# Kernel optimization log

Hardware: AMD Instinct MI355X
Metric: run time of the kernel (lower is better)

## Reference

```python
import jax, jax.numpy as jnp
import numpy as np

S, B, D = 2048, 2, 2048      # seq, batch, hidden  (x is [S, B, D])
H, KV, HD = 16, 4, 128        # n_head, n_kv_head, head_dim
N_REP = H // KV               # GQA repeat factor
THETA = 10000.0


def setup_inputs() -> dict:
    key = jax.random.key(0)
    ks = jax.random.split(key, 5)
    sc = 1.0 / np.sqrt(D)
    x = jax.random.normal(ks[0], (S, B, D), jnp.float32)
    Wq = jax.random.normal(ks[1], (D, H * HD), jnp.float32) * sc
    Wk = jax.random.normal(ks[2], (D, KV * HD), jnp.float32) * sc
    Wv = jax.random.normal(ks[3], (D, KV * HD), jnp.float32) * sc
    Wo = jax.random.normal(ks[4], (H * HD, D), jnp.float32) * sc
    return {"x": x, "Wq": Wq, "Wk": Wk, "Wv": Wv, "Wo": Wo}


def _rope_cos_sin(seq_len, dim, theta):
    inv_freq = 1.0 / (theta ** (jnp.arange(0, dim, 2, dtype=jnp.float32) / dim))
    t = jnp.arange(seq_len, dtype=jnp.float32)
    freqs = jnp.outer(t, inv_freq)                  # [S, dim/2]
    emb = jnp.concatenate([freqs, freqs], axis=-1)  # [S, dim]
    return jnp.cos(emb), jnp.sin(emb)


def _rotate_half(u):
    u1, u2 = jnp.split(u, 2, axis=-1)
    return jnp.concatenate([-u2, u1], axis=-1)


def reference(x, Wq, Wk, Wv, Wo):
    # projections (torch Linear without bias; W stored as [in, out] here)
    q = (x @ Wq).reshape(S, B, H, HD)
    k = (x @ Wk).reshape(S, B, KV, HD)
    v = (x @ Wv).reshape(S, B, KV, HD)

    # RoPE (full rotary, partial_rotary_factor == 1.0)
    cos, sin = _rope_cos_sin(S, HD, THETA)
    cos = cos[:, None, None, :]  # [S,1,1,HD] broadcasts over B, heads
    sin = sin[:, None, None, :]
    q = q * cos + _rotate_half(q) * sin
    k = k * cos + _rotate_half(k) * sin

    # GQA: repeat_interleave kv heads to match query heads
    k = jnp.repeat(k, N_REP, axis=2)
    v = jnp.repeat(v, N_REP, axis=2)

    # [S,B,H,HD] -> [B,H,S,HD]
    q = q.transpose(1, 2, 0, 3)
    k = k.transpose(1, 2, 0, 3)
    v = v.transpose(1, 2, 0, 3)

    # causal SDPA (dropout_p = 0 in eval)
    scale = 1.0 / np.sqrt(HD)
    scores = jnp.einsum('bhqd,bhkd->bhqk', q, k) * scale
    causal = jnp.tril(jnp.ones((S, S), dtype=bool))
    scores = jnp.where(causal, scores, jnp.finfo(scores.dtype).min)
    probs = jax.nn.softmax(scores, axis=-1)
    out = jnp.einsum('bhqk,bhkd->bhqd', probs, v)

    # [B,H,S,HD] -> [S,B,D], then output projection
    out = out.transpose(2, 0, 1, 3).reshape(S, B, D)
    return out @ Wo
```

## Files before the change

### kernel.cpp

```cpp
#include <hip/hip_runtime.h>
#include <hip/hip_bf16.h>
#include <cstdint>
#include <math.h>

#define S_LEN   2048
#define B_SZ    2
#define D_MODEL 2048
#define NH      16
#define NKV     4
#define HD      128
#define ROWS    (S_LEN * B_SZ)
#define NQKV    3072
#define SCALE   0.08838834764831845f

typedef __attribute__((ext_vector_type(8))) short short8;
typedef __attribute__((ext_vector_type(4))) float f32x4;

__device__ __forceinline__ short f2bf(float f) {
  union { float f; unsigned u; } v; v.f = f;
  unsigned r = v.u + 0x7fffu + ((v.u >> 16) & 1u);
  return (short)(r >> 16);
}
__device__ __forceinline__ float bf2f(short x) {
  union { unsigned u; float f; } v;
  v.u = ((unsigned)(unsigned short)x) << 16;
  return v.f;
}

__device__ __forceinline__ void async16(const short* g, short* l) {
  __builtin_amdgcn_global_load_lds(
      (const __attribute__((address_space(1))) void*)(uintptr_t)(const void*)g,
      (__attribute__((address_space(3))) void*)(uintptr_t)(void*)l,
      16, 0, 0);
}

template<int N> __device__ __forceinline__ void vm_wait() {
  asm volatile("s_waitcnt vmcnt(%0)" :: "n"(N) : "memory");
}

__global__ void cvt_bf16_kernel(const float* __restrict__ src, short* __restrict__ dst, int n4) {
  int t = blockIdx.x * blockDim.x + threadIdx.x;
  if (t >= n4) return;
  float4 v = ((const float4*)src)[t];
  short4 o;
  o.x = f2bf(v.x); o.y = f2bf(v.y); o.z = f2bf(v.z); o.w = f2bf(v.w);
  *(short4*)(dst + (size_t)t * 4) = o;
}

__global__ void wtrans_qkv_kernel(const float* __restrict__ Wq,
                                  const float* __restrict__ Wk,
                                  const float* __restrict__ Wv,
                                  short* __restrict__ dst) {
  __shared__ float tile[32][33];
  const int bx = blockIdx.x;
  const float* src;
  int Ndim, n0, drow;
  if (bx < 64)      { src = Wq; Ndim = 2048; n0 = bx * 32;        drow = n0; }
  else if (bx < 80) { src = Wk; Ndim = 512;  n0 = (bx - 64) * 32; drow = 2048 + n0; }
  else              { src = Wv; Ndim = 512;  n0 = (bx - 80) * 32; drow = 2560 + n0; }
  const int k0 = blockIdx.y * 32;
  for (int r = threadIdx.y; r < 32; r += 8)
    tile[r][threadIdx.x] = src[(size_t)(k0 + r) * Ndim + n0 + threadIdx.x];
  __syncthreads();
  for (int r = threadIdx.y; r < 32; r += 8)
    dst[(size_t)(drow + r) * 2048 + k0 + threadIdx.x] = f2bf(tile[threadIdx.x][r]);
}

__global__ void wtrans_kernel(const float* __restrict__ src, short* __restrict__ dst,
                              int Kdim, int Ndim) {
  __shared__ float tile[32][33];
  int n0 = blockIdx.x * 32, k0 = blockIdx.y * 32;
  for (int r = threadIdx.y; r < 32; r += 8)
    tile[r][threadIdx.x] = src[(size_t)(k0 + r) * Ndim + n0 + threadIdx.x];
  __syncthreads();
  for (int r = threadIdx.y; r < 32; r += 8)
    dst[(size_t)(n0 + r) * Kdim + k0 + threadIdx.x] = f2bf(tile[threadIdx.x][r]);
}

template<int BM, int BF16OUT>
__global__ __launch_bounds__(512, 2) void gemm3_kernel(const short* __restrict__ A,
    const short* __restrict__ Bt, void* __restrict__ Cv, int N, int K) {
  constexpr int MGRP  = BM / 16;
  constexpr int MI    = BM / 32;
  constexpr int NP    = MI / 2;
  constexpr int BCALLS = 4;
  constexpr int ACALLS = MGRP / 4;
  constexpr int CALLS = BCALLS + ACALLS;
  constexpr int BS_SH = 16384;
  constexpr int BUFSH = BS_SH + MGRP * 1024;
  __shared__ alignas(16) short lds[2 * BUFSH];

  const int tid  = threadIdx.x;
  const int w    = tid >> 6, lane = tid & 63;
  const int quad = lane >> 4, lr = lane & 15;
  const int wm   = w >> 2, wn = w & 3;

  const int nwg = gridDim.x;
  const int id  = (blockIdx.x & 7) * (nwg >> 3) + (blockIdx.x >> 3);
  const int nbx = N >> 8;
  const int bx = id % nbx, by = id / nbx;
  const int m0 = by * BM, n0 = bx * 256;

  const short* gsrc[CALLS];
  int dsts[CALLS];
#pragma unroll
  for (int c = 0; c < CALLS; ++c) {
    if (c < BCALLS) {
      const int sb = c * 8 + w, ng = sb >> 1, kk = sb & 1;
      gsrc[c] = Bt + (size_t)(n0 + ng * 16 + lr) * K + kk * 32 + quad * 8;
      dsts[c] = sb * 512;
    } else {
      const int p = c - BCALLS;
      const int mg = (w >> 2) * (MGRP / 2) + 2 * p + ((w >> 1) & 1), kk = w & 1;
      gsrc[c] = A + (size_t)(m0 + mg * 16 + lr) * K + kk * 32 + quad * 8;
      dsts[c] = BS_SH + (p * 8 + w) * 512;
    }
  }

  f32x4 acc[MI][4];
#pragma unroll
  for (int i = 0; i < MI; ++i)
#pragma unroll
    for (int j = 0; j < 4; ++j) acc[i][j] = (f32x4){0.f, 0.f, 0.f, 0.f};

  auto stage = [&](int t, int c) {
    async16(gsrc[c] + (size_t)t * 64, lds + (t & 1) * BUFSH + dsts[c]);
  };

  const int NT = K >> 6;
#pragma unroll
  for (int c = 0; c < CALLS; ++c) stage(0, c);
  if (BM == 256) vm_wait<3>(); else vm_wait<1>();
  __builtin_amdgcn_s_barrier();
  asm volatile("" ::: "memory");

  for (int t = 0; t < NT; ++t) {
    const short* lb = lds + (t & 1) * BUFSH;
    const bool pre = (t + 1) < NT;
    short8 b[4][2];
#pragma unroll
    for (int p = 0; p < NP; ++p) {
      if (p == 0) {
#pragma unroll
        for (int j = 0; j < 4; ++j)
#pragma unroll
          for (int kk = 0; kk < 2; ++kk)
            b[j][kk] = *(const short8*)(lb + ((wn * 4 + j) * 2 + kk) * 512 + lane * 8);
      }
      short8 a[2][2];
#pragma unroll
      for (int e = 0; e < 2; ++e)
#pragma unroll
        for (int kk = 0; kk < 2; ++kk)
          a[e][kk] = *(const short8*)(lb + BS_SH + (p * 8 + (wm * 2 + e) * 2 + kk) * 512 + lane * 8);
      if (pre) {
        if (NP == 4) { stage(t + 1, 2 * p); stage(t + 1, 2 * p + 1); }
        else         { stage(t + 1, 3 * p); stage(t + 1, 3 * p + 1); stage(t + 1, 3 * p + 2); }
      }
      asm volatile("" ::: "memory");
      __builtin_amdgcn_s_barrier();
      asm volatile("s_waitcnt lgkmcnt(0)" ::: "memory");
      __builtin_amdgcn_s_setprio(1);
#pragma unroll
      for (int kk = 0; kk < 2; ++kk)
#pragma unroll
        for (int e = 0; e < 2; ++e)
#pragma unroll
          for (int j = 0; j < 4; ++j)
            acc[2 * p + e][j] = __builtin_amdgcn_mfma_f32_16x16x32_bf16(a[e][kk], b[j][kk], acc[2 * p + e][j], 0, 0, 0);
      __builtin_amdgcn_s_setprio(0);
      if (pre) {
        if (NP == 4) {
          if (p == 0) vm_wait<4>(); else if (p == 1) vm_wait<5>();
          else if (p == 2) vm_wait<6>(); else vm_wait<3>();
        } else {
          if (p == 0) vm_wait<3>(); else vm_wait<1>();
        }
      } else {
        if (NP == 4) {
          if (p == 0) vm_wait<2>(); else if (p == 1) vm_wait<1>();
          else if (p == 2) vm_wait<0>();
        } else {
          if (p == 0) vm_wait<0>();
        }
      }
      asm volatile("" ::: "memory");
      __builtin_amdgcn_s_barrier();
      asm volatile("" ::: "memory");
    }
  }

#pragma unroll
  for (int i = 0; i < MI; ++i) {
    const int row = m0 + wm * (BM / 2) + i * 16 + quad * 4;
#pragma unroll
    for (int j = 0; j < 4; ++j) {
      const int col = n0 + wn * 64 + j * 16 + lr;
#pragma unroll
      for (int r = 0; r < 4; ++r) {
        const float v = acc[i][j][r];
        if (BF16OUT) ((short*)Cv)[(size_t)(row + r) * N + col] = f2bf(v);
        else         ((float*)Cv)[(size_t)(row + r) * N + col] = v;
      }
    }
  }
}

__global__ void rope_kernel(const short* __restrict__ QKVb, short* __restrict__ Qb,
                            short* __restrict__ Kpack) {
  const int head = blockIdx.y;
  const int t = blockIdx.x * blockDim.x + threadIdx.x;
  const int i = t & 63;
  const int row = t >> 6;
  const int s = row >> 1;
  const int b = row & 1;
  float inv_freq = __expf(-(float)i * (1.0f / 64.0f) * 9.210340371976184f);
  float ang = (float)s * inv_freq;
  float sn, cs;
  __sincosf(ang, &sn, &cs);
  if (head < NH) {
    const short* p = QKVb + (size_t)row * NQKV + head * HD;
    float v1 = bf2f(p[i]), v2 = bf2f(p[i + 64]);
    short* q = Qb + ((size_t)(b * NH + head) * S_LEN + s) * HD;
    q[i]      = f2bf((v1 * cs - v2 * sn) * SCALE);
    q[i + 64] = f2bf((v2 * cs + v1 * sn) * SCALE);
  } else {
    const int kv = head - NH;
    const short* p = QKVb + (size_t)row * NQKV + NH * HD + kv * HD;
    float v1 = bf2f(p[i]), v2 = bf2f(p[i + 64]);
    float k1 = v1 * cs - v2 * sn;
    float k2 = v2 * cs + v1 * sn;
    short* kp = Kpack + (size_t)(b * NKV + kv) * S_LEN * HD;
    const int tile = s >> 4, lrr = s & 15;
    const int d1 = i, d2 = i + 64;
    kp[(size_t)((tile * 4 + (d1 >> 5)) * 64 + ((d1 >> 3) & 3) * 16 + lrr) * 8 + (d1 & 7)] = f2bf(k1);
    kp[(size_t)((tile * 4 + (d2 >> 5)) * 64 + ((d2 >> 3) & 3) * 16 + lrr) * 8 + (d2 & 7)] = f2bf(k2);
  }
}

__global__ void vpack_kernel(const short* __restrict__ QKVb, short* __restrict__ Vpack) {
  __shared__ short tile[32][136];
  const int tid = threadIdx.x;
  const int chunk = blockIdx.x & 63, stream = blockIdx.x >> 6;
  const int b = stream >> 2, kv = stream & 3;
  const int vcol = NH * HD + NKV * HD + kv * HD;
  {
    const int r = tid >> 3, c = (tid & 7) * 16;
    const short* src = QKVb + (size_t)((chunk * 32 + r) * B_SZ + b) * NQKV + vcol + c;
    *(short8*)(&tile[r][c])     = *(const short8*)(src);
    *(short8*)(&tile[r][c + 8]) = *(const short8*)(src + 8);
  }
  __syncthreads();
  const int wave = tid >> 6, lane = tid & 63, quad = lane >> 4, lr = lane & 15;
  short* dst = Vpack + (size_t)stream * HD * S_LEN + chunk * 4096 + lane * 8;
#pragma unroll
  for (int k = 0; k < 2; ++k) {
    const int dt = wave + k * 4;
    short8 v;
#pragma unroll
    for (int j = 0; j < 8; ++j) v[j] = tile[quad * 8 + j][dt * 16 + lr];
    *(short8*)(dst + dt * 512) = v;
  }
}

#define PSP 72

template<bool MASK>
__device__ __forceinline__ void attn_iter64(
    const short* __restrict__ Ks, const short* __restrict__ Vs,
    short* __restrict__ Psw, const short8 qf[4], int kv0, int nt, int qlim,
    int quad, int lr, int lane, f32x4 o[8], float& m_i, float& l_i)
{
  const int lane_off = lane * 8;
  f32x4 sc[4];
#pragma unroll
  for (int t = 0; t < 4; ++t) {
    if (t < nt) {
      const short* kp = Ks + t * 2048 + lane_off;
      f32x4 s = (f32x4){0.f, 0.f, 0.f, 0.f};
#pragma unroll
      for (int c = 0; c < 4; ++c) {
        short8 kf = *(const short8*)(kp + c * 512);
        s = __builtin_amdgcn_mfma_f32_16x16x32_bf16(kf, qf[c], s, 0, 0, 0);
      }
      sc[t] = s;
    } else {
      sc[t] = (f32x4){-3.0e38f, -3.0e38f, -3.0e38f, -3.0e38f};
    }
  }
  if (MASK) {
#pragma unroll
    for (int t = 0; t < 4; ++t)
#pragma unroll
      for (int r = 0; r < 4; ++r)
        if (kv0 + t * 16 + quad * 4 + r > qlim) sc[t][r] = -3.0e38f;
  }
  float mb = -3.0e38f;
#pragma unroll
  for (int t = 0; t < 4; ++t)
#pragma unroll
    for (int r = 0; r < 4; ++r) mb = fmaxf(mb, sc[t][r]);
  mb = fmaxf(mb, __shfl_xor(mb, 16, 64));
  mb = fmaxf(mb, __shfl_xor(mb, 32, 64));
  const float mnew = fmaxf(m_i, mb);
  const float alpha = __expf(m_i - mnew);
  m_i = mnew;
  float rs = 0.f;
#pragma unroll
  for (int t = 0; t < 4; ++t) {
    float p0 = __expf(sc[t][0] - mnew);
    float p1 = __expf(sc[t][1] - mnew);
    float p2 = __expf(sc[t][2] - mnew);
    float p3 = __expf(sc[t][3] - mnew);
    rs += (p0 + p1) + (p2 + p3);
    __hip_bfloat162 pk01 = __float22bfloat162_rn(make_float2(p0, p1));
    __hip_bfloat162 pk23 = __float22bfloat162_rn(make_float2(p2, p3));
    __hip_bfloat162* pd = (__hip_bfloat162*)(Psw + lr * PSP + t * 16 + quad * 4);
    pd[0] = pk01;
    pd[1] = pk23;
  }
  rs += __shfl_xor(rs, 16, 64);
  rs += __shfl_xor(rs, 32, 64);
  l_i = l_i * alpha + rs;
#pragma unroll
  for (int n = 0; n < 8; ++n)
#pragma unroll
    for (int r = 0; r < 4; ++r) o[n][r] *= alpha;
  short8 pb0 = *(const short8*)(Psw + lr * PSP + quad * 8);
#pragma unroll
  for (int dt = 0; dt < 8; ++dt) {
    short8 vf = *(const short8*)(Vs + dt * 512 + lane_off);
    o[dt] = __builtin_amdgcn_mfma_f32_16x16x32_bf16(vf, pb0, o[dt], 0, 0, 0);
  }
  if (!MASK || nt > 2) {
    short8 pb1 = *(const short8*)(Psw + lr * PSP + 32 + quad * 8);
#pragma unroll
    for (int dt = 0; dt < 8; ++dt) {
      short8 vf = *(const short8*)(Vs + 4096 + dt * 512 + lane_off);
      o[dt] = __builtin_amdgcn_mfma_f32_16x16x32_bf16(vf, pb1, o[dt], 0, 0, 0);
    }
  }
}

__global__ __launch_bounds__(256) void attn_kernel(const short* __restrict__ Qb,
    const short* __restrict__ Kpack, const short* __restrict__ Vpack,
    short* __restrict__ Ob) {
  __shared__ alignas(16) short Ks[2][64 * HD];
  __shared__ alignas(16) short Vs[2][64 * HD];
  __shared__ alignas(16) short Ps[4][16 * PSP];
  const int tid = threadIdx.x, wave = tid >> 6, lane = tid & 63;
  const int quad = lane >> 4, lr = lane & 15;
  const int bid = blockIdx.x;
  const int sid  = bid & 7;
  const int hsub = (bid >> 3) & 3;
  const int qg   = 31 - (bid >> 5);
  const int b = sid >> 2, kvh = sid & 3;
  const int h = kvh * 4 + hsub;
  const int qw = (qg * 4 + wave) * 16;

  const short* Qp  = Qb    + ((size_t)(b * NH + h) * S_LEN + qw) * HD;
  const short* Kpk = Kpack + (size_t)(b * NKV + kvh) * S_LEN * HD;
  const short* Vpk = Vpack + (size_t)(b * NKV + kvh) * HD * S_LEN;
  short* Psw = &Ps[wave][0];

  short8 qf[4];
#pragma unroll
  for (int c = 0; c < 4; ++c)
    qf[c] = *(const short8*)(Qp + lr * HD + c * 32 + quad * 8);

  f32x4 o[8];
#pragma unroll
  for (int n = 0; n < 8; ++n) o[n] = (f32x4){0.f, 0.f, 0.f, 0.f};
  float m_i = -3.0e38f, l_i = 0.f;

  auto stage_kv = [&](int it) {
    const int buf = it & 1;
    const int kv0 = it * 64;
    const short* gk = Kpk + (size_t)kv0 * HD;
    const short* gv = Vpk + (size_t)(kv0 >> 5) * 4096;
#pragma unroll
    for (int k = 0; k < 4; ++k) {
      const int off = (wave * 4 + k) * 512;
      async16(gk + off + lane * 8, &Ks[buf][off]);
      async16(gv + off + lane * 8, &Vs[buf][off]);
    }
  };

  const int qlim = qw + lr;
  stage_kv(0);
  for (int it = 0; it <= qg; ++it) {
    __syncthreads();
    if (it < qg) stage_kv(it + 1);
    const int buf = it & 1;
    if (it < qg)
      attn_iter64<false>(Ks[buf], Vs[buf], Psw, qf, it * 64, 4, qlim, quad, lr, lane, o, m_i, l_i);
    else
      attn_iter64<true>(Ks[buf], Vs[buf], Psw, qf, it * 64, wave + 1, qlim, quad, lr, lane, o, m_i, l_i);
  }

  const float invl = 1.0f / l_i;
  short* op = Ob + ((size_t)(qw + lr) * B_SZ + b) * D_MODEL + h * HD + quad * 4;
#pragma unroll
  for (int dt = 0; dt < 8; ++dt) {
    short4 ov;
    ov.x = f2bf(o[dt][0] * invl);
    ov.y = f2bf(o[dt][1] * invl);
    ov.z = f2bf(o[dt][2] * invl);
    ov.w = f2bf(o[dt][3] * invl);
    *(short4*)(op + dt * 16) = ov;
  }
}

extern "C" void kernel_launch(void* const* d_in, const int* in_sizes, int n_in,
                              void* d_out, int out_size, void* d_ws, size_t ws_size,
                              hipStream_t stream) {
  (void)in_sizes; (void)n_in; (void)out_size; (void)ws_size;
  const float* x  = (const float*)d_in[0];
  const float* Wq = (const float*)d_in[1];
  const float* Wk = (const float*)d_in[2];
  const float* Wv = (const float*)d_in[3];
  const float* Wo = (const float*)d_in[4];
  float* out = (float*)d_out;
  char* ws = (char*)d_ws;

  short* Wqkv_t = (short*)(ws);
  short* xb     = (short*)(ws + 12582912);
  short* Qb     = (short*)(ws);
  short* Kpack  = (short*)(ws + 16777216);
  short* Vpack  = (short*)(ws + 25165824);
  short* QKVb   = (short*)(ws + 29360128);
  short* Ob     = (short*)(ws + 29360128);
  short* Wo_t   = (short*)(ws + 54525952);

  dim3 tblk(32, 8);

  cvt_bf16_kernel<<<(ROWS * D_MODEL / 4 + 255) / 256, 256, 0, stream>>>(x, xb, ROWS * D_MODEL / 4);
  wtrans_qkv_kernel<<<dim3(96, 64), tblk, 0, stream>>>(Wq, Wk, Wv, Wqkv_t);
  wtrans_kernel<<<dim3(64, 64), tblk, 0, stream>>>(Wo, Wo_t, 2048, 2048);
  gemm3_kernel<256, 1><<<dim3((NQKV / 256) * (ROWS / 256)), 512, 0, stream>>>(xb, Wqkv_t, QKVb, NQKV, D_MODEL);
  rope_kernel<<<dim3(1024, NH + NKV), 256, 0, stream>>>(QKVb, Qb, Kpack);
  vpack_kernel<<<dim3(512), 256, 0, stream>>>(QKVb, Vpack);
  attn_kernel<<<dim3(1024), 256, 0, stream>>>(Qb, Kpack, Vpack, Ob);
  gemm3_kernel<128, 0><<<dim3((D_MODEL / 256) * (ROWS / 128)), 512, 0, stream>>>(Ob, Wo_t, out, D_MODEL, D_MODEL);
}
```

Before: 338.2 us.

## Generalize GEMM tile width, skip softmax rescale, single-buffer attention KV

The GEMM kernel is templated on the N tile width, and the QKV projection now uses 192-wide tiles so the grid has 256 workgroups instead of 192 on the 256-CU part. Wait counts for the async loads are now computed generically. In attention, the online-softmax rescale of the accumulator is skipped when no lane's running max increases. The KV double buffering is replaced by a single buffer with load-then-sync, which halves LDS use but drops the overlap between loads and compute.

```diff
diff --git a/kernel.cpp b/kernel.cpp
--- a/kernel.cpp
+++ b/kernel.cpp
@@ -36,6 +36,15 @@
 
 template<int N> __device__ __forceinline__ void vm_wait() {
   asm volatile("s_waitcnt vmcnt(%0)" :: "n"(N) : "memory");
+}
+
+__host__ __device__ constexpr int sw_steady(int p, int ACALLS, int CALLS, int ISS) {
+  int a = ACALLS - p - 2; if (a < 0) a = 0;
+  int b = (p + 1) * ISS;  if (b > CALLS) b = CALLS;
+  return a + b;
+}
+__host__ __device__ constexpr int sw_last(int p, int ACALLS) {
+  int a = ACALLS - p - 2; return a < 0 ? 0 : a;
 }
 
 __global__ void cvt_bf16_kernel(const float* __restrict__ src, short* __restrict__ dst, int n4) {
@@ -77,16 +86,19 @@
     dst[(size_t)(n0 + r) * Kdim + k0 + threadIdx.x] = f2bf(tile[threadIdx.x][r]);
 }
 
-template<int BM, int BF16OUT>
+template<int BM, int BN, int BF16OUT>
 __global__ __launch_bounds__(512, 2) void gemm3_kernel(const short* __restrict__ A,
     const short* __restrict__ Bt, void* __restrict__ Cv, int N, int K) {
   constexpr int MGRP  = BM / 16;
   constexpr int MI    = BM / 32;
   constexpr int NP    = MI / 2;
-  constexpr int BCALLS = 4;
+  constexpr int NGRP  = BN / 16;
+  constexpr int NJ    = BN / 64;
+  constexpr int BCALLS = NGRP / 4;
   constexpr int ACALLS = MGRP / 4;
   constexpr int CALLS = BCALLS + ACALLS;
-  constexpr int BS_SH = 16384;
+  constexpr int ISS   = (NP == 4) ? 2 : 3;
+  constexpr int BS_SH = NGRP * 1024;
   constexpr int BUFSH = BS_SH + MGRP * 1024;
   __shared__ alignas(16) short lds[2 * BUFSH];
 
@@ -97,9 +109,9 @@
 
   const int nwg = gridDim.x;
   const int id  = (blockIdx.x & 7) * (nwg >> 3) + (blockIdx.x >> 3);
-  const int nbx = N >> 8;
+  const int nbx = N / BN;
   const int bx = id % nbx, by = id / nbx;
-  const int m0 = by * BM, n0 = bx * 256;
+  const int m0 = by * BM, n0 = bx * BN;
 
   const short* gsrc[CALLS];
   int dsts[CALLS];
@@ -117,11 +129,11 @@
     }
   }
 
-  f32x4 acc[MI][4];
+  f32x4 acc[MI][NJ];
 #pragma unroll
   for (int i = 0; i < MI; ++i)
 #pragma unroll
-    for (int j = 0; j < 4; ++j) acc[i][j] = (f32x4){0.f, 0.f, 0.f, 0.f};
+    for (int j = 0; j < NJ; ++j) acc[i][j] = (f32x4){0.f, 0.f, 0.f, 0.f};
 
   auto stage = [&](int t, int c) {
     async16(gsrc[c] + (size_t)t * 64, lds + (t & 1) * BUFSH + dsts[c]);
@@ -130,22 +142,22 @@
   const int NT = K >> 6;
 #pragma unroll
   for (int c = 0; c < CALLS; ++c) stage(0, c);
-  if (BM == 256) vm_wait<3>(); else vm_wait<1>();
+  vm_wait<ACALLS - 1>();
   __builtin_amdgcn_s_barrier();
   asm volatile("" ::: "memory");
 
   for (int t = 0; t < NT; ++t) {
     const short* lb = lds + (t & 1) * BUFSH;
     const bool pre = (t + 1) < NT;
-    short8 b[4][2];
+    short8 b[NJ][2];
 #pragma unroll
     for (int p = 0; p < NP; ++p) {
       if (p == 0) {
 #pragma unroll
-        for (int j = 0; j < 4; ++j)
+        for (int j = 0; j < NJ; ++j)
 #pragma unroll
           for (int kk = 0; kk < 2; ++kk)
-            b[j][kk] = *(const short8*)(lb + ((wn * 4 + j) * 2 + kk) * 512 + lane * 8);
+            b[j][kk] = *(const short8*)(lb + ((wn * NJ + j) * 2 + kk) * 512 + lane * 8);
       }
       short8 a[2][2];
 #pragma unroll
@@ -154,8 +166,9 @@
         for (int kk = 0; kk < 2; ++kk)
           a[e][kk] = *(const short8*)(lb + BS_SH + (p * 8 + (wm * 2 + e) * 2 + kk) * 512 + lane * 8);
       if (pre) {
-        if (NP == 4) { stage(t + 1, 2 * p); stage(t + 1, 2 * p + 1); }
-        else         { stage(t + 1, 3 * p); stage(t + 1, 3 * p + 1); stage(t + 1, 3 * p + 2); }
+#pragma unroll
+        for (int c = p * ISS; c < ((p + 1) * ISS < CALLS ? (p + 1) * ISS : CALLS); ++c)
+          stage(t + 1, c);
       }
       asm volatile("" ::: "memory");
       __builtin_amdgcn_s_barrier();
@@ -166,23 +179,18 @@
 #pragma unroll
         for (int e = 0; e < 2; ++e)
 #pragma unroll
-          for (int j = 0; j < 4; ++j)
+          for (int j = 0; j < NJ; ++j)
             acc[2 * p + e][j] = __builtin_amdgcn_mfma_f32_16x16x32_bf16(a[e][kk], b[j][kk], acc[2 * p + e][j], 0, 0, 0);
       __builtin_amdgcn_s_setprio(0);
       if (pre) {
-        if (NP == 4) {
-          if (p == 0) vm_wait<4>(); else if (p == 1) vm_wait<5>();
-          else if (p == 2) vm_wait<6>(); else vm_wait<3>();
-        } else {
-          if (p == 0) vm_wait<3>(); else vm_wait<1>();
-        }
+        if (p == NP - 1)      vm_wait<ACALLS - 1>();
+        else if (p == 0)      vm_wait<sw_steady(0, ACALLS, CALLS, ISS)>();
+        else if (p == 1)      vm_wait<sw_steady(1, ACALLS, CALLS, ISS)>();
+        else if (p == 2)      vm_wait<sw_steady(2, ACALLS, CALLS, ISS)>();
       } else {
-        if (NP == 4) {
-          if (p == 0) vm_wait<2>(); else if (p == 1) vm_wait<1>();
-          else if (p == 2) vm_wait<0>();
-        } else {
-          if (p == 0) vm_wait<0>();
-        }
+        if (p == 0 && NP > 1)      vm_wait<sw_last(0, ACALLS)>();
+        else if (p == 1 && NP > 2) vm_wait<sw_last(1, ACALLS)>();
+        else if (p == 2 && NP > 3) vm_wait<sw_last(2, ACALLS)>();
       }
       asm volatile("" ::: "memory");
       __builtin_amdgcn_s_barrier();
@@ -194,8 +202,8 @@
   for (int i = 0; i < MI; ++i) {
     const int row = m0 + wm * (BM / 2) + i * 16 + quad * 4;
 #pragma unroll
-    for (int j = 0; j < 4; ++j) {
-      const int col = n0 + wn * 64 + j * 16 + lr;
+    for (int j = 0; j < NJ; ++j) {
+      const int col = n0 + wn * (16 * NJ) + j * 16 + lr;
 #pragma unroll
       for (int r = 0; r < 4; ++r) {
         const float v = acc[i][j][r];
@@ -302,16 +310,23 @@
     for (int r = 0; r < 4; ++r) mb = fmaxf(mb, sc[t][r]);
   mb = fmaxf(mb, __shfl_xor(mb, 16, 64));
   mb = fmaxf(mb, __shfl_xor(mb, 32, 64));
-  const float mnew = fmaxf(m_i, mb);
-  const float alpha = __expf(m_i - mnew);
-  m_i = mnew;
+  if (!__all(mb <= m_i)) {
+    const float mnew = fmaxf(m_i, mb);
+    const float alpha = __expf(m_i - mnew);
+    m_i = mnew;
+    l_i *= alpha;
+#pragma unroll
+    for (int n = 0; n < 8; ++n)
+#pragma unroll
+      for (int r = 0; r < 4; ++r) o[n][r] *= alpha;
+  }
   float rs = 0.f;
 #pragma unroll
   for (int t = 0; t < 4; ++t) {
-    float p0 = __expf(sc[t][0] - mnew);
-    float p1 = __expf(sc[t][1] - mnew);
-    float p2 = __expf(sc[t][2] - mnew);
-    float p3 = __expf(sc[t][3] - mnew);
+    float p0 = __expf(sc[t][0] - m_i);
+    float p1 = __expf(sc[t][1] - m_i);
+    float p2 = __expf(sc[t][2] - m_i);
+    float p3 = __expf(sc[t][3] - m_i);
     rs += (p0 + p1) + (p2 + p3);
     __hip_bfloat162 pk01 = __float22bfloat162_rn(make_float2(p0, p1));
     __hip_bfloat162 pk23 = __float22bfloat162_rn(make_float2(p2, p3));
@@ -321,11 +336,7 @@
   }
   rs += __shfl_xor(rs, 16, 64);
   rs += __shfl_xor(rs, 32, 64);
-  l_i = l_i * alpha + rs;
-#pragma unroll
-  for (int n = 0; n < 8; ++n)
-#pragma unroll
-    for (int r = 0; r < 4; ++r) o[n][r] *= alpha;
+  l_i += rs;
   short8 pb0 = *(const short8*)(Psw + lr * PSP + quad * 8);
 #pragma unroll
   for (int dt = 0; dt < 8; ++dt) {
@@ -345,8 +356,8 @@
 __global__ __launch_bounds__(256) void attn_kernel(const short* __restrict__ Qb,
     const short* __restrict__ Kpack, const short* __restrict__ Vpack,
     short* __restrict__ Ob) {
-  __shared__ alignas(16) short Ks[2][64 * HD];
-  __shared__ alignas(16) short Vs[2][64 * HD];
+  __shared__ alignas(16) short Ks[64 * HD];
+  __shared__ alignas(16) short Vs[64 * HD];
   __shared__ alignas(16) short Ps[4][16 * PSP];
   const int tid = threadIdx.x, wave = tid >> 6, lane = tid & 63;
   const int quad = lane >> 4, lr = lane & 15;
@@ -373,29 +384,25 @@
   for (int n = 0; n < 8; ++n) o[n] = (f32x4){0.f, 0.f, 0.f, 0.f};
   float m_i = -3.0e38f, l_i = 0.f;
 
-  auto stage_kv = [&](int it) {
-    const int buf = it & 1;
+  const int qlim = qw + lr;
+  for (int it = 0; it <= qg; ++it) {
     const int kv0 = it * 64;
-    const short* gk = Kpk + (size_t)kv0 * HD;
-    const short* gv = Vpk + (size_t)(kv0 >> 5) * 4096;
-#pragma unroll
-    for (int k = 0; k < 4; ++k) {
-      const int off = (wave * 4 + k) * 512;
-      async16(gk + off + lane * 8, &Ks[buf][off]);
-      async16(gv + off + lane * 8, &Vs[buf][off]);
-    }
-  };
-
-  const int qlim = qw + lr;
-  stage_kv(0);
-  for (int it = 0; it <= qg; ++it) {
     __syncthreads();
-    if (it < qg) stage_kv(it + 1);
-    const int buf = it & 1;
+    {
+      const short* gk = Kpk + (size_t)kv0 * HD;
+      const short* gv = Vpk + (size_t)(kv0 >> 5) * 4096;
+#pragma unroll
+      for (int k = 0; k < 4; ++k) {
+        const int off = (wave * 4 + k) * 512;
+        async16(gk + off + lane * 8, Ks + off);
+        async16(gv + off + lane * 8, Vs + off);
+      }
+    }
+    __syncthreads();
     if (it < qg)
-      attn_iter64<false>(Ks[buf], Vs[buf], Psw, qf, it * 64, 4, qlim, quad, lr, lane, o, m_i, l_i);
+      attn_iter64<false>(Ks, Vs, Psw, qf, kv0, 4, qlim, quad, lr, lane, o, m_i, l_i);
     else
-      attn_iter64<true>(Ks[buf], Vs[buf], Psw, qf, it * 64, wave + 1, qlim, quad, lr, lane, o, m_i, l_i);
+      attn_iter64<true>(Ks, Vs, Psw, qf, kv0, wave + 1, qlim, quad, lr, lane, o, m_i, l_i);
   }
 
   const float invl = 1.0f / l_i;
@@ -437,9 +444,9 @@
   cvt_bf16_kernel<<<(ROWS * D_MODEL / 4 + 255) / 256, 256, 0, stream>>>(x, xb, ROWS * D_MODEL / 4);
   wtrans_qkv_kernel<<<dim3(96, 64), tblk, 0, stream>>>(Wq, Wk, Wv, Wqkv_t);
   wtrans_kernel<<<dim3(64, 64), tblk, 0, stream>>>(Wo, Wo_t, 2048, 2048);
-  gemm3_kernel<256, 1><<<dim3((NQKV / 256) * (ROWS / 256)), 512, 0, stream>>>(xb, Wqkv_t, QKVb, NQKV, D_MODEL);
+  gemm3_kernel<256, 192, 1><<<dim3((NQKV / 192) * (ROWS / 256)), 512, 0, stream>>>(xb, Wqkv_t, QKVb, NQKV, D_MODEL);
   rope_kernel<<<dim3(1024, NH + NKV), 256, 0, stream>>>(QKVb, Qb, Kpack);
   vpack_kernel<<<dim3(512), 256, 0, stream>>>(QKVb, Vpack);
   attn_kernel<<<dim3(1024), 256, 0, stream>>>(Qb, Kpack, Vpack, Ob);
-  gemm3_kernel<128, 0><<<dim3((D_MODEL / 256) * (ROWS / 128)), 512, 0, stream>>>(Ob, Wo_t, out, D_MODEL, D_MODEL);
-}
+  gemm3_kernel<128, 256, 0><<<dim3((D_MODEL / 256) * (ROWS / 128)), 512, 0, stream>>>(Ob, Wo_t, out, D_MODEL, D_MODEL);
+}
```

Measured after the change: 324.3 us. -4.1%, faster.
